# Optimization experiments

Hardware: AMD Instinct MI355X
Metric: run time of the kernel (lower is better)

## Reference

```python
import jax, jax.numpy as jnp
import numpy as np

# hyperparameters from init_kwargs
TEMP = 0.05
MOMENTUM = 0.2
ALPHA = 0.9
TEMP_DIST = 0.6
LAMBDA1 = 1.0
LAMBDA2 = 1.0
EPS_CONS = 2.0
NUM_SAMPLES = 8192
NUM_FEATURES = 2048
B = 256
K = 20
EPS = 1e-12


def setup_inputs() -> dict:
    key = jax.random.key(0)
    ks = jax.random.split(key, 8)
    inputs0 = jax.random.normal(ks[0], (B, NUM_FEATURES), dtype=jnp.float32)
    logits0 = jax.random.normal(ks[1], (B, NUM_SAMPLES), dtype=jnp.float32)
    logits1 = jax.random.normal(ks[2], (B, NUM_SAMPLES), dtype=jnp.float32)
    targets = jax.random.randint(ks[3], (B,), 0, NUM_SAMPLES, dtype=jnp.int32)
    indexes = jnp.arange(B, dtype=jnp.int32)  # global idx == batch idx (identity idx2bidx)
    neighbors = jax.random.randint(ks[4], (B, K), 0, B, dtype=jnp.int32)
    neighbor_dists = jax.random.uniform(ks[5], (B, K), dtype=jnp.float32)
    rampup = jnp.ones((), dtype=jnp.float32)
    features = jax.random.normal(ks[6], (NUM_SAMPLES, NUM_FEATURES), dtype=jnp.float32)
    features = features / jnp.linalg.norm(features, axis=1, keepdims=True)
    return {
        'inputs0': inputs0, 'logits0': logits0, 'logits1': logits1,
        'targets': targets, 'indexes': indexes, 'neighbors': neighbors,
        'neighbor_dists': neighbor_dists, 'rampup': rampup, 'features': features,
    }


def reference(inputs0, logits0, logits1, targets, indexes, neighbors,
              neighbor_dists, rampup, features):
    # F.normalize(inputs[0], dim=1)
    x = inputs0 / jnp.maximum(jnp.linalg.norm(inputs0, axis=1, keepdims=True), EPS)

    # CM forward: scores against memory bank, scaled by temperature
    outputs = (x @ features.T) / TEMP                      # [B, S]
    logp = jax.nn.log_softmax(outputs, axis=-1)
    loss_nce = -jnp.mean(jnp.take_along_axis(logp, targets[:, None], axis=1))

    targets_onehot = jax.nn.one_hot(targets, NUM_SAMPLES, dtype=logits0.dtype)

    # neighbor gathering: indexes = arange(B) so idx2bidx is identity; every
    # neighbor in [0,B) passes the `nb in indexes` filter.
    p0 = jax.nn.softmax(logits0, axis=-1)[neighbors]       # [B, K, S]
    p1 = jax.nn.softmax(logits1, axis=-1)[neighbors]       # [B, K, S]
    # loop appends logits0-row then logits1-row per neighbor -> interleave
    p = jnp.stack([p0, p1], axis=2).reshape(B, 2 * K, NUM_SAMPLES)
    d2 = jnp.repeat(neighbor_dists, 2, axis=1)             # [B, 2K] (d,d pairs)
    w = jax.nn.softmax(d2 / TEMP_DIST, axis=1)             # [B, 2K]
    logits_neighbors1 = jnp.einsum('bk,bks->bs', w, p)     # [B, S]

    # KL branch: neighbors with dist <= eps_consistency (all, since eps=2.0)
    mask = (neighbor_dists <= EPS_CONS).astype(p0.dtype)   # [B, K]
    cnt = jnp.maximum(mask.sum(axis=1, keepdims=True), 1.0)
    logits_neighbors1_KL = jnp.einsum('bk,bks->bs', mask, p0) / cnt  # [B, S]

    refined = ALPHA * targets_onehot + (1.0 - ALPHA) * jax.lax.stop_gradient(logits_neighbors1)
    loss_ce = jnp.mean(jnp.sum(-refined * jax.nn.log_softmax(logits0, axis=-1), axis=1))

    # KLDivLoss(logsoftmax(logits1).detach(), target) with batchmean reduction
    lp1 = jax.lax.stop_gradient(jax.nn.log_softmax(logits1, axis=-1))
    t = logits_neighbors1_KL
    kl = jnp.sum(jnp.where(t > 0, t * (jnp.log(jnp.maximum(t, EPS)) - lp1), 0.0)) / B

    # CM momentum memory-bank scatter update (backward side-effect in torch);
    # equivalent to the sequential loop when targets are unique in the batch.
    upd = MOMENTUM * features[targets] + (1.0 - MOMENTUM) * x
    upd = upd / jnp.maximum(jnp.linalg.norm(upd, axis=1, keepdims=True), EPS)
    new_features = features.at[targets].set(upd)

    return (loss_nce, LAMBDA1 * loss_ce, LAMBDA2 * rampup * kl, new_features)
```

## Files before the change

### kernel.cpp

```cpp
#include <hip/hip_runtime.h>
#include <cmath>

#define NB 256
#define NS 8192
#define NF 2048
#define NK 20

typedef _Float16 half8 __attribute__((ext_vector_type(8)));
typedef _Float16 half4 __attribute__((ext_vector_type(4)));
typedef float f32x4 __attribute__((ext_vector_type(4)));

__device__ __forceinline__ void async16(const void* g, void* l) {
  __builtin_amdgcn_global_load_lds(
      (const __attribute__((address_space(1))) unsigned int*)g,
      (__attribute__((address_space(3))) unsigned int*)l, 16, 0, 0);
}

__device__ __forceinline__ float waveSum(float v) {
#pragma unroll
  for (int off = 32; off > 0; off >>= 1) v += __shfl_xor(v, off, 64);
  return v;
}
__device__ __forceinline__ float waveMax(float v) {
#pragma unroll
  for (int off = 32; off > 0; off >>= 1) v = fmaxf(v, __shfl_xor(v, off, 64));
  return v;
}

__global__ __launch_bounds__(256, 1) void prep(
    const float* __restrict__ in0, const float* __restrict__ logits0,
    const float* __restrict__ logits1, const int* __restrict__ neighbors,
    const float* __restrict__ ndist, _Float16* __restrict__ Pt,
    _Float16* __restrict__ xh, _Float16* __restrict__ alpha_h,
    float* __restrict__ mll, _Float16* __restrict__ Wp,
    float* __restrict__ loss) {
  __shared__ alignas(16) union {
    struct {
      float redA[4];
      float redB[4];
    } s;
    _Float16 Lt[16 * 520];
  } sm;
  int tid = threadIdx.x, blk = blockIdx.x;
  int wave = tid >> 6, lane = tid & 63;

  if (blk < 512) {
    if (blk == 0 && tid < 3) loss[tid] = 0.0f;
    int r = blk;
    const float* src = (r < NB) ? logits0 : logits1;
    const float4* row = (const float4*)(src + (size_t)(r & (NB - 1)) * NS);
    float4 v[8];
    float mx = -1e30f;
#pragma unroll
    for (int i = 0; i < 8; ++i) {
      v[i] = row[tid + i * 256];
      mx = fmaxf(mx, fmaxf(fmaxf(v[i].x, v[i].y), fmaxf(v[i].z, v[i].w)));
    }
    float wv = waveMax(mx);
    if (lane == 0) sm.s.redA[wave] = wv;
    __syncthreads();
    float m = fmaxf(fmaxf(sm.s.redA[0], sm.s.redA[1]), fmaxf(sm.s.redA[2], sm.s.redA[3]));
    float se = 0.0f;
#pragma unroll
    for (int i = 0; i < 8; ++i)
      se += expf(v[i].x - m) + expf(v[i].y - m) + expf(v[i].z - m) + expf(v[i].w - m);
    float sw = waveSum(se);
    if (lane == 0) sm.s.redB[wave] = sw;
    __syncthreads();
    float l = (sm.s.redB[0] + sm.s.redB[1]) + (sm.s.redB[2] + sm.s.redB[3]);
    if (tid == 0) {
      mll[r] = m + logf(l);
      alpha_h[r] = (_Float16)(256.0f * expf(-m) / l);
    }
  } else if (blk < 1024) {
    int s0 = (blk - 512) * 16;
#pragma unroll
    for (int g = 0; g < 8; ++g) {
      int pos = g * 256 + tid;
      int row = pos >> 2, c4 = pos & 3;
      const float* src = ((row < NB) ? logits0 + (size_t)row * NS
                                     : logits1 + (size_t)(row - NB) * NS) + s0 + c4 * 4;
      float4 v = *(const float4*)src;
      sm.Lt[(c4 * 4 + 0) * 520 + row] = (_Float16)expf(v.x);
      sm.Lt[(c4 * 4 + 1) * 520 + row] = (_Float16)expf(v.y);
      sm.Lt[(c4 * 4 + 2) * 520 + row] = (_Float16)expf(v.z);
      sm.Lt[(c4 * 4 + 3) * 520 + row] = (_Float16)expf(v.w);
    }
    __syncthreads();
    int srow = tid >> 4, seg = tid & 15;
    _Float16* dst = Pt + (size_t)(s0 + srow) * 512 + seg * 32;
    const _Float16* lsrc = &sm.Lt[srow * 520 + seg * 32];
#pragma unroll
    for (int q = 0; q < 4; ++q)
      *(half8*)(dst + q * 8) = *(const half8*)(lsrc + q * 8);
  } else if (blk < 1280) {
    int b = blk - 1024;
    const float4* row = (const float4*)(in0 + (size_t)b * NF);
    float4 v0 = row[tid], v1 = row[tid + 256];
    float ss = v0.x * v0.x + v0.y * v0.y + v0.z * v0.z + v0.w * v0.w +
               v1.x * v1.x + v1.y * v1.y + v1.z * v1.z + v1.w * v1.w;
    float w = waveSum(ss);
    if (lane == 0) sm.s.redA[wave] = w;
    __syncthreads();
    float tot = (sm.s.redA[0] + sm.s.redA[1]) + (sm.s.redA[2] + sm.s.redA[3]);
    float inv = 1.0f / fmaxf(sqrtf(tot), 1e-12f);
    half4 h0, h1;
    h0[0] = (_Float16)(v0.x * inv); h0[1] = (_Float16)(v0.y * inv);
    h0[2] = (_Float16)(v0.z * inv); h0[3] = (_Float16)(v0.w * inv);
    h1[0] = (_Float16)(v1.x * inv); h1[1] = (_Float16)(v1.y * inv);
    h1[2] = (_Float16)(v1.z * inv); h1[3] = (_Float16)(v1.w * inv);
    ((half4*)(xh + (size_t)b * NF))[tid] = h0;
    ((half4*)(xh + (size_t)b * NF))[tid + 256] = h1;
  } else {
    int b = blk - 1280;
    _Float16* rkl = Wp + (size_t)b * 512;
    _Float16* rce = Wp + (size_t)(256 + b) * 512;
    if (tid < 64) ((float4*)rkl)[tid] = make_float4(0, 0, 0, 0);
    else if (tid < 128) ((float4*)rce)[tid - 64] = make_float4(0, 0, 0, 0);
    __syncthreads();
    if (tid == 0) {
      float d[NK], e[NK];
      int n[NK];
      float s = 0.0f;
      int cnt = 0;
#pragma unroll
      for (int k = 0; k < NK; ++k) {
        d[k] = ndist[b * NK + k];
        n[k] = neighbors[b * NK + k];
        e[k] = expf(d[k] * (1.0f / 0.6f));
        s += e[k];
        cnt += (d[k] <= 2.0f) ? 1 : 0;
      }
      float invs = 1.0f / (2.0f * s);
      float invc = 1.0f / fmaxf((float)cnt, 1.0f);
#pragma unroll
      for (int k = 0; k < NK; ++k) {
        bool first = true;
#pragma unroll
        for (int k2 = 0; k2 < NK; ++k2)
          if (k2 < k && n[k2] == n[k]) first = false;
        if (first) {
          float wsum = 0.0f, ksum = 0.0f;
#pragma unroll
          for (int k2 = 0; k2 < NK; ++k2)
            if (k2 >= k && n[k2] == n[k]) {
              wsum += e[k2] * invs;
              ksum += (d[k2] <= 2.0f) ? invc : 0.0f;
            }
          rkl[n[k]] = (_Float16)ksum;
          rce[n[k]] = (_Float16)wsum;
          rce[256 + n[k]] = (_Float16)wsum;
        }
      }
    }
  }
}

__global__ __launch_bounds__(256) void gemms(
    const _Float16* __restrict__ xh, const float* __restrict__ fB,
    const _Float16* __restrict__ Wp, const _Float16* __restrict__ Pt,
    const _Float16* __restrict__ alpha_h,
    const float* __restrict__ logits0, const float* __restrict__ logits1,
    const float* __restrict__ mll, const int* __restrict__ targets,
    float* __restrict__ outF, float* __restrict__ pm, float* __restrict__ pl,
    float* __restrict__ tgt, float* __restrict__ part) {
  __shared__ alignas(16) _Float16 As[128 * 128];
  __shared__ alignas(16) _Float16 Bs[128 * 64];
  __shared__ alignas(16) _Float16 Al[512];
  __shared__ float red[4];
  int tid = threadIdx.x, wave = tid >> 6, lane = tid & 63;
  int quad = lane >> 4, r16 = lane & 15, lrow = lane >> 3, lch = lane & 7;
  int blk = blockIdx.x;
  if (blk < 256) {
    int bx = blk & 127, by = blk >> 7;
    int n0 = bx * 64, m0 = by * 128;
    int rr = tid >> 4, cc = tid & 15;
    f32x4 acc[2][4] = {};
    for (int k0 = 0; k0 < NF; k0 += 128) {
      __syncthreads();
      float4 bv[4][2];
#pragma unroll
      for (int ss = 0; ss < 4; ++ss) {
        int row = ss * 16 + rr;
        int sc = cc ^ (row & 7);
        const float* src = fB + (size_t)(n0 + row) * NF + k0 + sc * 8;
        bv[ss][0] = *(const float4*)src;
        bv[ss][1] = *(const float4*)(src + 4);
      }
#pragma unroll
      for (int ss = 0; ss < 8; ++ss) {
        int row = ss * 16 + rr;
        int sc = cc ^ (row & 7);
        async16(xh + (size_t)(m0 + row) * NF + k0 + sc * 8, &As[row * 128 + cc * 8]);
      }
      bool doStore = (by == ((k0 >= NF / 2) ? 1 : 0));
#pragma unroll
      for (int ss = 0; ss < 4; ++ss) {
        int row = ss * 16 + rr;
        int sc = cc ^ (row & 7);
        half8 h;
        h[0] = (_Float16)bv[ss][0].x; h[1] = (_Float16)bv[ss][0].y;
        h[2] = (_Float16)bv[ss][0].z; h[3] = (_Float16)bv[ss][0].w;
        h[4] = (_Float16)bv[ss][1].x; h[5] = (_Float16)bv[ss][1].y;
        h[6] = (_Float16)bv[ss][1].z; h[7] = (_Float16)bv[ss][1].w;
        *(half8*)&Bs[row * 128 + cc * 8] = h;
        if (doStore) {
          float4* o = (float4*)(outF + (size_t)(n0 + row) * NF + k0 + sc * 8);
          o[0] = bv[ss][0];
          o[1] = bv[ss][1];
        }
      }
      __syncthreads();
#pragma unroll
      for (int sub = 0; sub < 4; ++sub) {
        int slot = ((sub * 4 + quad) ^ (r16 & 7)) * 8;
        half8 af[2], bf[4];
#pragma unroll
        for (int i = 0; i < 2; ++i)
          af[i] = *(const half8*)&As[(wave * 32 + i * 16 + r16) * 128 + slot];
#pragma unroll
        for (int j = 0; j < 4; ++j)
          bf[j] = *(const half8*)&Bs[(j * 16 + r16) * 128 + slot];
#pragma unroll
        for (int i = 0; i < 2; ++i)
#pragma unroll
          for (int j = 0; j < 4; ++j)
            acc[i][j] = __builtin_amdgcn_mfma_f32_16x16x32_f16(af[i], bf[j], acc[i][j], 0, 0, 0);
      }
    }
#pragma unroll
    for (int i = 0; i < 2; ++i)
#pragma unroll
      for (int r = 0; r < 4; ++r) {
        int R = m0 + wave * 32 + i * 16 + quad * 4 + r;
        float sv[4];
#pragma unroll
        for (int j = 0; j < 4; ++j) sv[j] = acc[i][j][r] * 20.0f;
        float mx = fmaxf(fmaxf(sv[0], sv[1]), fmaxf(sv[2], sv[3]));
#pragma unroll
        for (int m2 = 1; m2 < 16; m2 <<= 1) mx = fmaxf(mx, __shfl_xor(mx, m2, 64));
        float e = expf(sv[0] - mx) + expf(sv[1] - mx) + expf(sv[2] - mx) + expf(sv[3] - mx);
#pragma unroll
        for (int m2 = 1; m2 < 16; m2 <<= 1) e += __shfl_xor(e, m2, 64);
        int tg = targets[R];
#pragma unroll
        for (int j = 0; j < 4; ++j)
          if (n0 + j * 16 + r16 == tg) tgt[R] = sv[j];
        if (r16 == 0) { pm[R * 128 + bx] = mx; pl[R * 128 + bx] = e; }
      }
  } else {
    int nb = blk - 256;
    int bx = nb & 63, by = nb >> 6;
    int n0 = bx * 128, m0 = by * 128;
    int wm = (wave >> 1) * 64, wn = (wave & 1) * 64;
    if (tid < 64) ((half8*)Al)[tid] = ((const half8*)alpha_h)[tid];
    f32x4 acc[4][4] = {};
    for (int k0 = 0; k0 < 512; k0 += 64) {
      __syncthreads();
#pragma unroll
      for (int ss = 0; ss < 4; ++ss) {
        int rl = ss * 32 + wave * 8 + lrow;
        int sc = lch ^ (rl & 7);
        async16(Wp + (size_t)(m0 + rl) * 512 + k0 + sc * 8, &As[rl * 64 + lch * 8]);
        async16(Pt + (size_t)(n0 + rl) * 512 + k0 + sc * 8, &Bs[rl * 64 + lch * 8]);
      }
      __syncthreads();
#pragma unroll
      for (int sub = 0; sub < 2; ++sub) {
        int slot = ((sub * 4 + quad) ^ (r16 & 7)) * 8;
        half8 alv = *(const half8*)&Al[k0 + slot];
        half8 af[4], bf[4];
#pragma unroll
        for (int i = 0; i < 4; ++i)
          af[i] = *(const half8*)&As[(wm + i * 16 + r16) * 64 + slot];
#pragma unroll
        for (int j = 0; j < 4; ++j)
          bf[j] = *(const half8*)&Bs[(wn + j * 16 + r16) * 64 + slot] * alv;
#pragma unroll
        for (int i = 0; i < 4; ++i)
#pragma unroll
          for (int j = 0; j < 4; ++j)
            acc[i][j] = __builtin_amdgcn_mfma_f32_16x16x32_f16(af[i], bf[j], acc[i][j], 0, 0, 0);
      }
    }
    bool iskl = (by < 2);
    const float* lgbase = iskl ? logits1 : logits0;
    float local = 0.0f;
#pragma unroll
    for (int i = 0; i < 4; ++i)
#pragma unroll
      for (int r = 0; r < 4; ++r) {
        int Mg = m0 + wm + i * 16 + quad * 4 + r;
        int b = iskl ? Mg : (Mg - 256);
        float mv = mll[iskl ? 256 + b : b];
        const float* lgrow = lgbase + (size_t)b * NS + n0 + wn;
#pragma unroll
        for (int j = 0; j < 4; ++j) {
          float lg = lgrow[j * 16 + r16];
          float t = acc[i][j][r] * (1.0f / 256.0f);
          if (iskl)
            local += (t > 0.0f) ? t * (logf(fmaxf(t, 1e-12f)) - (lg - mv)) : 0.0f;
          else
            local += -0.1f * t * (lg - mv);
        }
      }
    float wsv = waveSum(local);
    if (lane == 0) red[wave] = wsv;
    __syncthreads();
    if (tid == 0) part[nb] = (red[0] + red[1]) + (red[2] + red[3]);
  }
}

__global__ __launch_bounds__(128) void final_reduce(
    const float* __restrict__ pm, const float* __restrict__ pl,
    const float* __restrict__ tgt, const float* __restrict__ part,
    const float* __restrict__ logits0, const float* __restrict__ mll,
    const int* __restrict__ targets, const float* __restrict__ rampup,
    const float* __restrict__ in0, const float* __restrict__ features,
    float* __restrict__ outF, float* __restrict__ out) {
  __shared__ float rA[2], rB[2];
  __shared__ int flag;
  int tid = threadIdx.x, blk = blockIdx.x;
  if (blk < 256) {
    int b = blk;
    float m = pm[b * 128 + tid];
    float l = pl[b * 128 + tid];
    float wm = waveMax(m);
    if ((tid & 63) == 0) rA[tid >> 6] = wm;
    __syncthreads();
    float mx = fmaxf(rA[0], rA[1]);
    float e = l * expf(m - mx);
    float ws = waveSum(e);
    if ((tid & 63) == 0) rB[tid >> 6] = ws;
    __syncthreads();
    if (tid == 0) {
      float S = rB[0] + rB[1];
      float nce = -(tgt[b] - mx - logf(S));
      int tg = targets[b];
      float oh = -0.9f * (logits0[(size_t)b * NS + tg] - mll[b]);
      float pb = part[b];
      float v1 = oh;
      if (b >= 128) v1 += pb;
      atomicAdd(out + 0, nce * (1.0f / 256.0f));
      atomicAdd(out + 1, v1 * (1.0f / 256.0f));
      if (b < 128) atomicAdd(out + 2, rampup[0] * pb * (1.0f / 256.0f));
    }
  } else {
    int b = blk - 256;
    int tg = targets[b];
    if (tid == 0) flag = 0;
    __syncthreads();
    bool later = false;
    for (int i = b + 1 + tid; i < 256; i += 128) later = later || (targets[i] == tg);
    if (later) flag = 1;
    __syncthreads();
    if (flag) return;
    const float4* xr = (const float4*)(in0 + (size_t)b * NF);
    const float4* fr = (const float4*)(features + (size_t)tg * NF);
    float4 a[4];
    float ssx = 0.0f;
#pragma unroll
    for (int s = 0; s < 4; ++s) {
      a[s] = xr[tid + s * 128];
      ssx += a[s].x * a[s].x + a[s].y * a[s].y + a[s].z * a[s].z + a[s].w * a[s].w;
    }
    float w1 = waveSum(ssx);
    if ((tid & 63) == 0) rA[tid >> 6] = w1;
    __syncthreads();
    float ix = 0.8f / fmaxf(sqrtf(rA[0] + rA[1]), 1e-12f);
    float4 v[4];
    float ss = 0.0f;
#pragma unroll
    for (int s = 0; s < 4; ++s) {
      float4 f = fr[tid + s * 128];
      v[s] = make_float4(0.2f * f.x + ix * a[s].x, 0.2f * f.y + ix * a[s].y,
                         0.2f * f.z + ix * a[s].z, 0.2f * f.w + ix * a[s].w);
      ss += v[s].x * v[s].x + v[s].y * v[s].y + v[s].z * v[s].z + v[s].w * v[s].w;
    }
    float w2 = waveSum(ss);
    if ((tid & 63) == 0) rB[tid >> 6] = w2;
    __syncthreads();
    float inv = 1.0f / fmaxf(sqrtf(rB[0] + rB[1]), 1e-12f);
    float4* o4 = (float4*)(outF + (size_t)tg * NF);
#pragma unroll
    for (int s = 0; s < 4; ++s)
      o4[tid + s * 128] = make_float4(v[s].x * inv, v[s].y * inv, v[s].z * inv, v[s].w * inv);
  }
}

extern "C" void kernel_launch(void* const* d_in, const int* in_sizes, int n_in,
                              void* d_out, int out_size, void* d_ws, size_t ws_size,
                              hipStream_t stream) {
  const float* inputs0 = (const float*)d_in[0];
  const float* logits0 = (const float*)d_in[1];
  const float* logits1 = (const float*)d_in[2];
  const int* targets = (const int*)d_in[3];
  const int* neighbors = (const int*)d_in[5];
  const float* ndist = (const float*)d_in[6];
  const float* rampup = (const float*)d_in[7];
  const float* features = (const float*)d_in[8];
  float* out = (float*)d_out;

  char* ws = (char*)d_ws;
  float* mll = (float*)(ws + 4096);
  _Float16* alpha_h = (_Float16*)(ws + 8192);
  float* part = (float*)(ws + 12288);
  float* tgt = (float*)(ws + 16384);
  float* pm = (float*)(ws + 65536);
  float* pl = (float*)(ws + 196608);
  _Float16* Wp = (_Float16*)(ws + 524288);
  _Float16* xh = (_Float16*)(ws + (3 << 20));
  _Float16* Pt = (_Float16*)(ws + (4 << 20));

  prep<<<1536, 256, 0, stream>>>(inputs0, logits0, logits1, neighbors, ndist,
                                 Pt, xh, alpha_h, mll, Wp, out);
  gemms<<<512, 256, 0, stream>>>(xh, features, Wp, Pt, alpha_h, logits0, logits1,
                                 mll, targets, out + 3, pm, pl, tgt, part);
  final_reduce<<<512, 128, 0, stream>>>(pm, pl, tgt, part, logits0, mll, targets,
                                        rampup, inputs0, features, out + 3, out);
}
```

Baseline: 195.7 us.

## Drop LDS staging in GEMMs, load MFMA fragments directly from global memory

```diff
diff --git a/kernel.cpp b/kernel.cpp
--- a/kernel.cpp
+++ b/kernel.cpp
@@ -9,12 +9,6 @@
 typedef _Float16 half8 __attribute__((ext_vector_type(8)));
 typedef _Float16 half4 __attribute__((ext_vector_type(4)));
 typedef float f32x4 __attribute__((ext_vector_type(4)));
-
-__device__ __forceinline__ void async16(const void* g, void* l) {
-  __builtin_amdgcn_global_load_lds(
-      (const __attribute__((address_space(1))) unsigned int*)g,
-      (__attribute__((address_space(3))) unsigned int*)l, 16, 0, 0);
-}
 
 __device__ __forceinline__ float waveSum(float v) {
 #pragma unroll
@@ -156,7 +150,7 @@
   }
 }
 
-__global__ __launch_bounds__(256) void gemms(
+__global__ __launch_bounds__(256, 3) void gemms(
     const _Float16* __restrict__ xh, const float* __restrict__ fB,
     const _Float16* __restrict__ Wp, const _Float16* __restrict__ Pt,
     const _Float16* __restrict__ alpha_h,
@@ -164,124 +158,90 @@
     const float* __restrict__ mll, const int* __restrict__ targets,
     float* __restrict__ outF, float* __restrict__ pm, float* __restrict__ pl,
     float* __restrict__ tgt, float* __restrict__ part) {
-  __shared__ alignas(16) _Float16 As[128 * 128];
-  __shared__ alignas(16) _Float16 Bs[128 * 64];
-  __shared__ alignas(16) _Float16 Al[512];
   __shared__ float red[4];
   int tid = threadIdx.x, wave = tid >> 6, lane = tid & 63;
-  int quad = lane >> 4, r16 = lane & 15, lrow = lane >> 3, lch = lane & 7;
+  int quad = lane >> 4, r16 = lane & 15;
   int blk = blockIdx.x;
   if (blk < 256) {
     int bx = blk & 127, by = blk >> 7;
     int n0 = bx * 64, m0 = by * 128;
-    int rr = tid >> 4, cc = tid & 15;
-    f32x4 acc[2][4] = {};
-    for (int k0 = 0; k0 < NF; k0 += 128) {
-      __syncthreads();
-      float4 bv[4][2];
-#pragma unroll
-      for (int ss = 0; ss < 4; ++ss) {
-        int row = ss * 16 + rr;
-        int sc = cc ^ (row & 7);
-        const float* src = fB + (size_t)(n0 + row) * NF + k0 + sc * 8;
-        bv[ss][0] = *(const float4*)src;
-        bv[ss][1] = *(const float4*)(src + 4);
-      }
-#pragma unroll
-      for (int ss = 0; ss < 8; ++ss) {
-        int row = ss * 16 + rr;
-        int sc = cc ^ (row & 7);
-        async16(xh + (size_t)(m0 + row) * NF + k0 + sc * 8, &As[row * 128 + cc * 8]);
-      }
-      bool doStore = (by == ((k0 >= NF / 2) ? 1 : 0));
-#pragma unroll
-      for (int ss = 0; ss < 4; ++ss) {
-        int row = ss * 16 + rr;
-        int sc = cc ^ (row & 7);
+    int wmr = m0 + (wave >> 1) * 64 + r16;
+    int wnc = n0 + (wave & 1) * 32 + r16;
+    const _Float16* pa[4];
+    const float* pb[2];
+#pragma unroll
+    for (int i = 0; i < 4; ++i) pa[i] = xh + (size_t)(wmr + i * 16) * NF + quad * 8;
+#pragma unroll
+    for (int j = 0; j < 2; ++j) pb[j] = fB + (size_t)(wnc + j * 16) * NF + quad * 8;
+    f32x4 acc[4][2] = {};
+#pragma unroll 2
+    for (int kk = 0; kk < NF; kk += 32) {
+      half8 af[4], bf[2];
+#pragma unroll
+      for (int j = 0; j < 2; ++j) {
+        float4 lo = *(const float4*)(pb[j] + kk);
+        float4 hi = *(const float4*)(pb[j] + kk + 4);
         half8 h;
-        h[0] = (_Float16)bv[ss][0].x; h[1] = (_Float16)bv[ss][0].y;
-        h[2] = (_Float16)bv[ss][0].z; h[3] = (_Float16)bv[ss][0].w;
-        h[4] = (_Float16)bv[ss][1].x; h[5] = (_Float16)bv[ss][1].y;
-        h[6] = (_Float16)bv[ss][1].z; h[7] = (_Float16)bv[ss][1].w;
-        *(half8*)&Bs[row * 128 + cc * 8] = h;
-        if (doStore) {
-          float4* o = (float4*)(outF + (size_t)(n0 + row) * NF + k0 + sc * 8);
-          o[0] = bv[ss][0];
-          o[1] = bv[ss][1];
-        }
-      }
-      __syncthreads();
-#pragma unroll
-      for (int sub = 0; sub < 4; ++sub) {
-        int slot = ((sub * 4 + quad) ^ (r16 & 7)) * 8;
-        half8 af[2], bf[4];
-#pragma unroll
-        for (int i = 0; i < 2; ++i)
-          af[i] = *(const half8*)&As[(wave * 32 + i * 16 + r16) * 128 + slot];
-#pragma unroll
-        for (int j = 0; j < 4; ++j)
-          bf[j] = *(const half8*)&Bs[(j * 16 + r16) * 128 + slot];
-#pragma unroll
-        for (int i = 0; i < 2; ++i)
-#pragma unroll
-          for (int j = 0; j < 4; ++j)
-            acc[i][j] = __builtin_amdgcn_mfma_f32_16x16x32_f16(af[i], bf[j], acc[i][j], 0, 0, 0);
-      }
-    }
-#pragma unroll
-    for (int i = 0; i < 2; ++i)
+        h[0] = (_Float16)lo.x; h[1] = (_Float16)lo.y;
+        h[2] = (_Float16)lo.z; h[3] = (_Float16)lo.w;
+        h[4] = (_Float16)hi.x; h[5] = (_Float16)hi.y;
+        h[6] = (_Float16)hi.z; h[7] = (_Float16)hi.w;
+        bf[j] = h;
+      }
+#pragma unroll
+      for (int i = 0; i < 4; ++i) af[i] = *(const half8*)(pa[i] + kk);
+#pragma unroll
+      for (int i = 0; i < 4; ++i)
+#pragma unroll
+        for (int j = 0; j < 2; ++j)
+          acc[i][j] = __builtin_amdgcn_mfma_f32_16x16x32_f16(af[i], bf[j], acc[i][j], 0, 0, 0);
+    }
+    int sx = bx * 2 + (wave & 1);
+#pragma unroll
+    for (int i = 0; i < 4; ++i)
 #pragma unroll
       for (int r = 0; r < 4; ++r) {
-        int R = m0 + wave * 32 + i * 16 + quad * 4 + r;
-        float sv[4];
-#pragma unroll
-        for (int j = 0; j < 4; ++j) sv[j] = acc[i][j][r] * 20.0f;
-        float mx = fmaxf(fmaxf(sv[0], sv[1]), fmaxf(sv[2], sv[3]));
+        int R = m0 + (wave >> 1) * 64 + i * 16 + quad * 4 + r;
+        float s0 = acc[i][0][r] * 20.0f, s1 = acc[i][1][r] * 20.0f;
+        float mx = fmaxf(s0, s1);
 #pragma unroll
         for (int m2 = 1; m2 < 16; m2 <<= 1) mx = fmaxf(mx, __shfl_xor(mx, m2, 64));
-        float e = expf(sv[0] - mx) + expf(sv[1] - mx) + expf(sv[2] - mx) + expf(sv[3] - mx);
+        float e = expf(s0 - mx) + expf(s1 - mx);
 #pragma unroll
         for (int m2 = 1; m2 < 16; m2 <<= 1) e += __shfl_xor(e, m2, 64);
         int tg = targets[R];
-#pragma unroll
-        for (int j = 0; j < 4; ++j)
-          if (n0 + j * 16 + r16 == tg) tgt[R] = sv[j];
-        if (r16 == 0) { pm[R * 128 + bx] = mx; pl[R * 128 + bx] = e; }
-      }
-  } else {
+        if (wnc == tg) tgt[R] = s0;
+        if (wnc + 16 == tg) tgt[R] = s1;
+        if (r16 == 0) { pm[R * 256 + sx] = mx; pl[R * 256 + sx] = e; }
+      }
+  } else if (blk < 512) {
     int nb = blk - 256;
     int bx = nb & 63, by = nb >> 6;
     int n0 = bx * 128, m0 = by * 128;
     int wm = (wave >> 1) * 64, wn = (wave & 1) * 64;
-    if (tid < 64) ((half8*)Al)[tid] = ((const half8*)alpha_h)[tid];
+    const _Float16* pa[4];
+    const _Float16* pb[4];
+#pragma unroll
+    for (int i = 0; i < 4; ++i)
+      pa[i] = Wp + (size_t)(m0 + wm + i * 16 + r16) * 512 + quad * 8;
+#pragma unroll
+    for (int j = 0; j < 4; ++j)
+      pb[j] = Pt + (size_t)(n0 + wn + j * 16 + r16) * 512 + quad * 8;
+    const _Float16* pal = alpha_h + quad * 8;
     f32x4 acc[4][4] = {};
-    for (int k0 = 0; k0 < 512; k0 += 64) {
-      __syncthreads();
-#pragma unroll
-      for (int ss = 0; ss < 4; ++ss) {
-        int rl = ss * 32 + wave * 8 + lrow;
-        int sc = lch ^ (rl & 7);
-        async16(Wp + (size_t)(m0 + rl) * 512 + k0 + sc * 8, &As[rl * 64 + lch * 8]);
-        async16(Pt + (size_t)(n0 + rl) * 512 + k0 + sc * 8, &Bs[rl * 64 + lch * 8]);
-      }
-      __syncthreads();
-#pragma unroll
-      for (int sub = 0; sub < 2; ++sub) {
-        int slot = ((sub * 4 + quad) ^ (r16 & 7)) * 8;
-        half8 alv = *(const half8*)&Al[k0 + slot];
-        half8 af[4], bf[4];
-#pragma unroll
-        for (int i = 0; i < 4; ++i)
-          af[i] = *(const half8*)&As[(wm + i * 16 + r16) * 64 + slot];
+#pragma unroll 2
+    for (int kk = 0; kk < 512; kk += 32) {
+      half8 alv = *(const half8*)(pal + kk);
+      half8 af[4], bf[4];
+#pragma unroll
+      for (int i = 0; i < 4; ++i) af[i] = *(const half8*)(pa[i] + kk);
+#pragma unroll
+      for (int j = 0; j < 4; ++j) bf[j] = *(const half8*)(pb[j] + kk) * alv;
+#pragma unroll
+      for (int i = 0; i < 4; ++i)
 #pragma unroll
         for (int j = 0; j < 4; ++j)
-          bf[j] = *(const half8*)&Bs[(wn + j * 16 + r16) * 64 + slot] * alv;
-#pragma unroll
-        for (int i = 0; i < 4; ++i)
-#pragma unroll
-          for (int j = 0; j < 4; ++j)
-            acc[i][j] = __builtin_amdgcn_mfma_f32_16x16x32_f16(af[i], bf[j], acc[i][j], 0, 0, 0);
-      }
+          acc[i][j] = __builtin_amdgcn_mfma_f32_16x16x32_f16(af[i], bf[j], acc[i][j], 0, 0, 0);
     }
     bool iskl = (by < 2);
     const float* lgbase = iskl ? logits1 : logits0;
@@ -308,6 +268,11 @@
     if (lane == 0) red[wave] = wsv;
     __syncthreads();
     if (tid == 0) part[nb] = (red[0] + red[1]) + (red[2] + red[3]);
+  } else {
+    int r0 = (blk - 512) * 32;
+    const float4* src = (const float4*)fB + (size_t)r0 * 512;
+    float4* dst = (float4*)outF + (size_t)r0 * 512;
+    for (int i = tid; i < 32 * 512; i += 256) dst[i] = src[i];
   }
 }
 
@@ -323,13 +288,13 @@
   int tid = threadIdx.x, blk = blockIdx.x;
   if (blk < 256) {
     int b = blk;
-    float m = pm[b * 128 + tid];
-    float l = pl[b * 128 + tid];
-    float wm = waveMax(m);
+    float m1 = pm[b * 256 + tid], m2v = pm[b * 256 + 128 + tid];
+    float l1 = pl[b * 256 + tid], l2v = pl[b * 256 + 128 + tid];
+    float wm = waveMax(fmaxf(m1, m2v));
     if ((tid & 63) == 0) rA[tid >> 6] = wm;
     __syncthreads();
     float mx = fmaxf(rA[0], rA[1]);
-    float e = l * expf(m - mx);
+    float e = l1 * expf(m1 - mx) + l2v * expf(m2v - mx);
     float ws = waveSum(e);
     if ((tid & 63) == 0) rB[tid >> 6] = ws;
     __syncthreads();
@@ -407,14 +372,14 @@
   float* part = (float*)(ws + 12288);
   float* tgt = (float*)(ws + 16384);
   float* pm = (float*)(ws + 65536);
-  float* pl = (float*)(ws + 196608);
-  _Float16* Wp = (_Float16*)(ws + 524288);
+  float* pl = (float*)(ws + 65536 + 262144);
+  _Float16* Wp = (_Float16*)(ws + (1 << 20));
   _Float16* xh = (_Float16*)(ws + (3 << 20));
   _Float16* Pt = (_Float16*)(ws + (4 << 20));
 
   prep<<<1536, 256, 0, stream>>>(inputs0, logits0, logits1, neighbors, ndist,
                                  Pt, xh, alpha_h, mll, Wp, out);
-  gemms<<<512, 256, 0, stream>>>(xh, features, Wp, Pt, alpha_h, logits0, logits1,
+  gemms<<<768, 256, 0, stream>>>(xh, features, Wp, Pt, alpha_h, logits0, logits1,
                                  mll, targets, out + 3, pm, pl, tgt, part);
   final_reduce<<<512, 128, 0, stream>>>(pm, pl, tgt, part, logits0, mll, targets,
                                         rampup, inputs0, features, out + 3, out);
```

New measurement: 244.9 us. 1.25x slower.
